# Kernel tuning notes

Measured on AMD Instinct MI355X. Metric: run time of the kernel, lower is better.

The kernel has to match this reference:

```python
import jax, jax.numpy as jnp
import numpy as np

EPS = 1e-05
HEADS = 4

def rms_norm(x, w):
    norm = jax.lax.rsqrt(jnp.mean(x * x, axis=-1, keepdims=True) + EPS)
    return x * norm * w

def setup_inputs() -> dict:
    key = jax.random.key(0)
    ks = jax.random.split(key, 10)
    B, Nt, Nf, C = 2, 4096, 4096, 256
    s = 0.02
    return {
        "t": jax.random.normal(ks[0], (B, Nt, C), jnp.float32),
        "f": jax.random.normal(ks[1], (B, Nf, C), jnp.float32),
        "norm_w": jnp.ones((C,), jnp.float32),
        "wq": jax.random.normal(ks[2], (C, C), jnp.float32) * s,
        "bq": jnp.zeros((C,), jnp.float32),
        "wkv": jax.random.normal(ks[3], (C, 2 * C), jnp.float32) * s,
        "bkv": jnp.zeros((2 * C,), jnp.float32),
        "wp": jax.random.normal(ks[4], (C, C), jnp.float32) * s,
        "bp": jnp.zeros((C,), jnp.float32),
    }

def reference(t, f, norm_w, wq, bq, wkv, bkv, wp, bp):
    B, Nt, C = t.shape
    Nf = f.shape[1]
    H = HEADS
    Dh = C // H
    scale = Dh ** -0.5
    tn = rms_norm(t, norm_w)
    fn = rms_norm(f, norm_w)
    q = (tn @ wq + bq).reshape(B, Nt, H, Dh)          # b t h d
    kv = fn @ wkv + bkv
    k, v = jnp.split(kv, 2, axis=-1)
    k = k.reshape(B, Nf, H, Dh)                        # b f h d
    v = v.reshape(B, Nf, H, Dh)
    attn = jnp.einsum('bthd,bfhd->bhtf', q, k) * scale
    attn = jax.nn.softmax(attn, axis=-1)
    out = jnp.einsum('bhtf,bfhd->bthd', attn, v).reshape(B, Nt, C)
    return out @ wp + bp + tn
```

## Files before the change

### kernel.cpp

```cpp
#include <hip/hip_runtime.h>

typedef __bf16 bf16;
typedef __bf16 bf16x4 __attribute__((ext_vector_type(4)));
typedef __bf16 bf16x8 __attribute__((ext_vector_type(8)));
typedef float f32x2 __attribute__((ext_vector_type(2)));
typedef float f32x4 __attribute__((ext_vector_type(4)));
typedef float f32x16 __attribute__((ext_vector_type(16)));

__device__ __forceinline__ f32x4 mfma16(bf16x8 a, bf16x8 b, f32x4 c) {
  return __builtin_amdgcn_mfma_f32_16x16x32_bf16(a, b, c, 0, 0, 0);
}
__device__ __forceinline__ f32x16 mfma32(bf16x8 a, bf16x8 b, f32x16 c) {
  return __builtin_amdgcn_mfma_f32_32x32x16_bf16(a, b, c, 0, 0, 0);
}

__device__ __forceinline__ unsigned pack2(float lo, float hi) {
  unsigned short a = __builtin_bit_cast(unsigned short, (bf16)lo);
  unsigned short b = __builtin_bit_cast(unsigned short, (bf16)hi);
  return ((unsigned)b << 16) | (unsigned)a;
}

__device__ __forceinline__ unsigned cvtpk(float lo, float hi) {
  unsigned r;
  asm("v_cvt_pk_bf16_f32 %0, %1, %2" : "=v"(r) : "v"(lo), "v"(hi));
  return r;
}

__device__ __forceinline__ void plane32swap(unsigned& a, unsigned& b) {
  asm volatile("v_permlane32_swap_b32 %0, %1" : "+v"(a), "+v"(b));
}

__device__ __forceinline__ f32x2 pk_add(f32x2 a, f32x2 b) {
  f32x2 d;
  asm("v_pk_add_f32 %0, %1, %2" : "=v"(d) : "v"(a), "v"(b));
  return d;
}

typedef __attribute__((address_space(3))) unsigned int lds_u32;
typedef __attribute__((address_space(1))) unsigned int glb_u32;
__device__ __forceinline__ void gld16(const bf16* g, bf16* l) {
  __builtin_amdgcn_global_load_lds((const glb_u32*)g, (lds_u32*)l, 16, 0, 0);
}

__global__ __launch_bounds__(256)
void prep_kernel(const float* __restrict__ t, const float* __restrict__ f,
                 const float* __restrict__ nw,
                 const float* __restrict__ wq, const float* __restrict__ wkv,
                 const float* __restrict__ wp,
                 bf16* __restrict__ tn, bf16* __restrict__ fn,
                 bf16* __restrict__ wqT, bf16* __restrict__ wkvT,
                 bf16* __restrict__ wpT)
{
  int b = blockIdx.x;
  if (b < 1024) {
    int e = b * 256 + threadIdx.x;
    const float* src; bf16* dst; int N; int idx;
    if (e < 65536)       { src = wq;  dst = wqT;  N = 256; idx = e; }
    else if (e < 196608) { src = wkv; dst = wkvT; N = 512; idx = e - 65536; }
    else                 { src = wp;  dst = wpT;  N = 256; idx = e - 196608; }
    int k = idx & 255;
    int n = idx >> 8;
    dst[idx] = (bf16)src[(size_t)k * N + n];
    return;
  }
  int wave = threadIdx.x >> 6;
  int lane = threadIdx.x & 63;
  int row = (b - 1024) * 4 + wave;
  const float* src;
  bf16* dst;
  if (row < 8192) {
    src = t + (size_t)row * 256;
    dst = tn + (size_t)row * 256;
  } else {
    int r2 = row - 8192;
    src = f + (size_t)r2 * 256;
    dst = fn + (size_t)r2 * 256;
  }
  float4 v = reinterpret_cast<const float4*>(src)[lane];
  float ss = v.x * v.x + v.y * v.y + v.z * v.z + v.w * v.w;
  #pragma unroll
  for (int m = 1; m < 64; m <<= 1) ss += __shfl_xor(ss, m);
  float nrm = rsqrtf(ss * (1.0f / 256.0f) + 1e-5f);
  float4 wv = reinterpret_cast<const float4*>(nw)[lane];
  bf16x4 o;
  o[0] = (bf16)(v.x * nrm * wv.x);
  o[1] = (bf16)(v.y * nrm * wv.y);
  o[2] = (bf16)(v.z * nrm * wv.z);
  o[3] = (bf16)(v.w * nrm * wv.w);
  *reinterpret_cast<bf16x4*>(dst + lane * 4) = o;
}

template<int MODE>
__device__ __forceinline__
void gemm_body(int bid, bf16 (*As)[264], bf16 (*Bs)[264],
               const bf16* __restrict__ A, const bf16* __restrict__ Wt,
               const float* __restrict__ bias, bf16* __restrict__ o0,
               bf16* __restrict__ o1, const bf16* __restrict__ resid,
               float* __restrict__ outf, int N)
{
  int tid = threadIdx.x;
  int wv = tid >> 6;
  int lane = tid & 63;
  int lr = lane & 15;
  int lk = (lane >> 4) * 8;
  int wm = wv >> 1, wn = wv & 1;
  int nb = N >> 6;
  int bm = bid / nb;
  int bn = bid - bm * nb;
  int row0 = bm * 64;
  int col0 = bn * 64;

  #pragma unroll
  for (int j = 0; j < 8; j++) {
    int idx = tid + 256 * j;
    int r = idx >> 5, ch = idx & 31;
    *reinterpret_cast<bf16x8*>(&As[r][ch * 8]) =
        *reinterpret_cast<const bf16x8*>(A + (size_t)(row0 + r) * 256 + ch * 8);
    *reinterpret_cast<bf16x8*>(&Bs[r][ch * 8]) =
        *reinterpret_cast<const bf16x8*>(Wt + (size_t)(col0 + r) * 256 + ch * 8);
  }
  __syncthreads();

  f32x4 acc[2][2] = {};
  #pragma unroll
  for (int k0 = 0; k0 < 256; k0 += 32) {
    bf16x8 a[2], b[2];
    #pragma unroll
    for (int mi = 0; mi < 2; mi++)
      a[mi] = *reinterpret_cast<const bf16x8*>(&As[wm * 32 + mi * 16 + lr][k0 + lk]);
    #pragma unroll
    for (int ni = 0; ni < 2; ni++)
      b[ni] = *reinterpret_cast<const bf16x8*>(&Bs[wn * 32 + ni * 16 + lr][k0 + lk]);
    #pragma unroll
    for (int mi = 0; mi < 2; mi++)
      #pragma unroll
      for (int ni = 0; ni < 2; ni++)
        acc[mi][ni] = mfma16(a[mi], b[ni], acc[mi][ni]);
  }

  int rb = (lane >> 4) * 4;
  int row0w = row0 + wm * 32;
  int col0w = col0 + wn * 32;
  #pragma unroll
  for (int mi = 0; mi < 2; mi++) {
    #pragma unroll
    for (int ni = 0; ni < 2; ni++) {
      int col = col0w + ni * 16 + lr;
      float bv = bias[col];
      #pragma unroll
      for (int r = 0; r < 4; r++) {
        int row = row0w + mi * 16 + rb + r;
        float val = acc[mi][ni][r] + bv;
        if (MODE == 0) {
          int b_ = row >> 12, tt = row & 4095;
          int h = col >> 6, d = col & 63;
          o0[(((size_t)(b_ * 4 + h)) * 4096 + tt) * 64 + d] = (bf16)val;
        } else if (MODE == 1) {
          int b_ = row >> 12, ff = row & 4095;
          if (col < 256) {
            int h = col >> 6, d = col & 63;
            o0[(((size_t)(b_ * 4 + h)) * 4096 + ff) * 64 + d] = (bf16)val;
          } else {
            int c = col - 256;
            int h = c >> 6, d = c & 63;
            o1[(((size_t)(b_ * 4 + h)) * 64 + d) * 4096 + ff] = (bf16)val;
          }
        } else {
          size_t idx = (size_t)row * 256 + col;
          outf[idx] = val + (float)resid[idx];
        }
      }
    }
  }
}

__global__ __launch_bounds__(256)
void gemm_qkv(const bf16* __restrict__ tn, const bf16* __restrict__ fn,
              const bf16* __restrict__ wqT, const bf16* __restrict__ wkvT,
              const float* __restrict__ bq, const float* __restrict__ bkv,
              bf16* __restrict__ q, bf16* __restrict__ k, bf16* __restrict__ vt)
{
  __shared__ bf16 As[64][264];
  __shared__ bf16 Bs[64][264];
  if (blockIdx.x < 512)
    gemm_body<0>(blockIdx.x, As, Bs, tn, wqT, bq, q, nullptr, nullptr, nullptr, 256);
  else
    gemm_body<1>(blockIdx.x - 512, As, Bs, fn, wkvT, bkv, k, vt, nullptr, nullptr, 512);
}

__global__ __launch_bounds__(256)
void gemm_out(const bf16* __restrict__ ao, const bf16* __restrict__ wpT,
              const float* __restrict__ bp, const bf16* __restrict__ resid,
              float* __restrict__ outf)
{
  __shared__ bf16 As[64][264];
  __shared__ bf16 Bs[64][264];
  gemm_body<2>(blockIdx.x, As, Bs, ao, wpT, bp, nullptr, nullptr, resid, outf, 256);
}

__global__ __launch_bounds__(256, 4)
void attn_kernel(const bf16* __restrict__ Q, const bf16* __restrict__ K,
                 const bf16* __restrict__ Vt, unsigned* __restrict__ Opart,
                 float* __restrict__ Lp)
{
  int bid = blockIdx.x;
  int bh = bid & 7;
  int qb = (bid >> 3) & 31;
  int FQ = bid >> 8;
  int wv = threadIdx.x >> 6;
  int lane = threadIdx.x & 63;
  int lq = lane & 31;
  int h32 = lane >> 5;

  const bf16* Qb = Q + ((size_t)bh * 4096 + qb * 128 + wv * 32) * 64;
  const bf16* Kb = K + (size_t)bh * 4096 * 64;
  const bf16* Vb = Vt + (size_t)bh * 64 * 4096;

  __shared__ bf16 stage[2][4096];

  const float qs = 0.125f * 1.44269504089f;
  bf16x8 qf[4];
  #pragma unroll
  for (int kc = 0; kc < 4; kc++) {
    qf[kc] = *reinterpret_cast<const bf16x8*>(Qb + (size_t)lq * 64 + kc * 16 + h32 * 8);
    #pragma unroll
    for (int i = 0; i < 8; i++) qf[kc][i] = (bf16)((float)qf[kc][i] * qs);
  }

  f32x16 oa[2] = {};
  f32x2 l2 = {0.f, 0.f};

  int fbeg = FQ * 512;

  int role = wv >> 1;
  int half = wv & 1;
  const bf16 *p0, *p1;
  if (role == 0) {
    p0 = Kb + (size_t)(fbeg + lq) * 64 + h32 * 8 + half * 32;
    p1 = p0 + 32 * 64;
  } else {
    p0 = Vb + (size_t)lane * 4096 + fbeg + half * 16;
    p1 = p0 + 32;
  }
  const int so  = role ? 8 : 16;
  const int adv = role ? 64 : 64 * 64;
  const int db0 = wv * 1024;

  const bf16* kL0 = &stage[0][0] + h32 * 256 + lq * 8;
  const bf16* kL1 = &stage[1][0] + h32 * 256 + lq * 8;
  const bf16* vL0 = &stage[0][2048] + h32 * 512 + lq * 8;
  const bf16* vL1 = &stage[1][2048] + h32 * 512 + lq * 8;

  auto STAGE = [&](bf16* sb, const bf16* p) {
    gld16(p,      sb + db0);
    gld16(p + so, sb + db0 + 512);
  };

  auto QK = [&](const bf16* kL) -> f32x16 {
    f32x16 z = {};
    f32x16 st = mfma32(*reinterpret_cast<const bf16x8*>(kL),        qf[0], z);
    st        = mfma32(*reinterpret_cast<const bf16x8*>(kL + 512),  qf[1], st);
    st        = mfma32(*reinterpret_cast<const bf16x8*>(kL + 1024), qf[2], st);
    st        = mfma32(*reinterpret_cast<const bf16x8*>(kL + 1536), qf[3], st);
    return st;
  };

  auto SMPV = [&](f32x16 st, const bf16* vL) {
    union { f32x2 p2[8]; float s[16]; } u;
    #pragma unroll
    for (int r = 0; r < 16; r++) u.s[r] = exp2f(st[r]);

    f32x2 a0 = pk_add(u.p2[0], u.p2[1]);
    f32x2 a1 = pk_add(u.p2[2], u.p2[3]);
    f32x2 a2 = pk_add(u.p2[4], u.p2[5]);
    f32x2 a3 = pk_add(u.p2[6], u.p2[7]);
    a0 = pk_add(a0, a1);
    a2 = pk_add(a2, a3);
    a0 = pk_add(a0, a2);
    l2 = pk_add(l2, a0);

    unsigned w[8];
    #pragma unroll
    for (int j = 0; j < 8; j++) w[j] = cvtpk(u.s[2 * j], u.s[2 * j + 1]);
    plane32swap(w[0], w[2]);
    plane32swap(w[1], w[3]);
    plane32swap(w[4], w[6]);
    plane32swap(w[5], w[7]);
    union { unsigned u4[4]; bf16x8 v; } ub0, ub1;
    ub0.u4[0] = w[0]; ub0.u4[1] = w[1]; ub0.u4[2] = w[2]; ub0.u4[3] = w[3];
    ub1.u4[0] = w[4]; ub1.u4[1] = w[5]; ub1.u4[2] = w[6]; ub1.u4[3] = w[7];

    oa[0] = mfma32(*reinterpret_cast<const bf16x8*>(vL),        ub0.v, oa[0]);
    oa[0] = mfma32(*reinterpret_cast<const bf16x8*>(vL + 1024), ub1.v, oa[0]);
    oa[1] = mfma32(*reinterpret_cast<const bf16x8*>(vL + 256),  ub0.v, oa[1]);
    oa[1] = mfma32(*reinterpret_cast<const bf16x8*>(vL + 1280), ub1.v, oa[1]);
  };

  STAGE(&stage[0][0], p0);
  STAGE(&stage[1][0], p1);
  asm volatile("" ::: "memory");

  #pragma unroll 1
  for (int u = 0; u < 8; ++u) {
    asm volatile("s_waitcnt vmcnt(0)" ::: "memory");
    __builtin_amdgcn_s_barrier();
    asm volatile("" ::: "memory");

    f32x16 sa = QK(kL0);
    f32x16 sb = QK(kL1);
    SMPV(sa, vL0);
    SMPV(sb, vL1);

    asm volatile("" ::: "memory");
    __builtin_amdgcn_s_barrier();
    asm volatile("" ::: "memory");

    p0 += adv;
    p1 += adv;
    STAGE(&stage[0][0], p0);
    STAGE(&stage[1][0], p1);
    asm volatile("" ::: "memory");
  }

  asm volatile("s_waitcnt vmcnt(0)" ::: "memory");

  float l = l2[0] + l2[1];
  float ltot;
  {
    unsigned x = __builtin_bit_cast(unsigned, l), y = x;
    plane32swap(x, y);
    ltot = __builtin_bit_cast(float, x) + __builtin_bit_cast(float, y);
  }

  int tile = qb * 4 + wv;
  unsigned* op = Opart + (((size_t)(FQ * 8 + bh) * 128 + tile) * 1024);
  #pragma unroll
  for (int db = 0; db < 2; db++)
    #pragma unroll
    for (int j = 0; j < 8; j++) {
      int r = 2 * j;
      int d = db * 32 + 2 * (j & 1) + 8 * (j >> 1) + 4 * h32;
      op[(d >> 1) * 32 + lq] = cvtpk(oa[db][r], oa[db][r + 1]);
    }
  if (h32 == 0)
    Lp[((size_t)FQ * 8 + bh) * 4096 + tile * 32 + lq] = ltot;
}

__global__ __launch_bounds__(256)
void merge_kernel(const unsigned* __restrict__ Op, const float* __restrict__ Lp,
                  bf16* __restrict__ AO)
{
  int bid = blockIdx.x;
  int bh = bid & 7;
  int tile = bid >> 3;
  int tid = threadIdx.x;
  int q = tid & 31;
  int c4 = tid >> 5;
  int row0 = tile * 32;

  float L = 0.f;
  #pragma unroll
  for (int p = 0; p < 8; p++)
    L += Lp[((size_t)p * 8 + bh) * 4096 + row0 + q];
  float inv = 1.f / L;

  __shared__ unsigned tl[32][33];
  float a0[4] = {}, a1[4] = {};
  #pragma unroll
  for (int p = 0; p < 8; p++) {
    const unsigned* src = Op + (((size_t)p * 8 + bh) * 128 + tile) * 1024;
    #pragma unroll
    for (int j = 0; j < 4; j++) {
      unsigned v = src[(c4 + j * 8) * 32 + q];
      a0[j] += (float)__builtin_bit_cast(bf16, (unsigned short)(v & 0xffff));
      a1[j] += (float)__builtin_bit_cast(bf16, (unsigned short)(v >> 16));
    }
  }
  #pragma unroll
  for (int j = 0; j < 4; j++)
    tl[q][c4 + j * 8] = pack2(a0[j] * inv, a1[j] * inv);
  __syncthreads();

  int q2 = tid >> 3;
  int dg = tid & 7;
  unsigned ov[4];
  #pragma unroll
  for (int i = 0; i < 4; i++) ov[i] = tl[q2][dg * 4 + i];
  int b_ = bh >> 2, hh = bh & 3;
  int row = row0 + q2;
  unsigned* dst = (unsigned*)(AO + ((size_t)b_ * 4096 + row) * 256 + hh * 64) + dg * 4;
  *reinterpret_cast<uint4*>(dst) = *reinterpret_cast<const uint4*>(ov);
}

extern "C" void kernel_launch(void* const* d_in, const int* in_sizes, int n_in,
                              void* d_out, int out_size, void* d_ws, size_t ws_size,
                              hipStream_t stream) {
  const float* t   = (const float*)d_in[0];
  const float* f   = (const float*)d_in[1];
  const float* nw  = (const float*)d_in[2];
  const float* wq  = (const float*)d_in[3];
  const float* bq  = (const float*)d_in[4];
  const float* wkv = (const float*)d_in[5];
  const float* bkv = (const float*)d_in[6];
  const float* wp  = (const float*)d_in[7];
  const float* bp  = (const float*)d_in[8];
  float* out = (float*)d_out;

  bf16* ws = (bf16*)d_ws;
  const size_t NTOK = 2097152;
  bf16* tn   = ws;
  bf16* fn   = ws + NTOK;
  bf16* q    = ws + 2 * NTOK;
  bf16* k    = ws + 3 * NTOK;
  bf16* vt   = ws + 4 * NTOK;
  bf16* ao   = fn;
  bf16* wqT  = ws + 5 * NTOK;
  bf16* wkvT = wqT + 65536;
  bf16* wpT  = wkvT + 131072;
  unsigned* opart = (unsigned*)(wpT + 65536);
  float* lp = (float*)(opart + (size_t)8 * 8 * 128 * 1024);

  prep_kernel<<<5120, 256, 0, stream>>>(t, f, nw, wq, wkv, wp, tn, fn, wqT, wkvT, wpT);
  gemm_qkv<<<1536, 256, 0, stream>>>(tn, fn, wqT, wkvT, bq, bkv, q, k, vt);
  attn_kernel<<<2048, 256, 0, stream>>>(q, k, vt, opart, lp);
  merge_kernel<<<1024, 256, 0, stream>>>(opart, lp, ao);
  gemm_out<<<512, 256, 0, stream>>>(ao, wpT, bp, tn, out);
}
```

Baseline: 100.0 us.

## Double-buffer K/V shared-memory staging to overlap global loads with compute

Shared staging grows from two to four buffers, split into two pairs that alternate. While one pair is consumed by QK/softmax/PV, the loads for the other pair stay in flight, and the wait becomes vmcnt(4) instead of vmcnt(0). This is meant to hide global-to-LDS load latency behind MFMA work, but it doubles LDS per block to 32KB, which may reduce occupancy under launch bounds of 4 blocks per CU.

```diff
diff --git a/kernel.cpp b/kernel.cpp
--- a/kernel.cpp
+++ b/kernel.cpp
@@ -216,7 +216,7 @@
   const bf16* Kb = K + (size_t)bh * 4096 * 64;
   const bf16* Vb = Vt + (size_t)bh * 64 * 4096;
 
-  __shared__ bf16 stage[2][4096];
+  __shared__ bf16 stage[4][4096];
 
   const float qs = 0.125f * 1.44269504089f;
   bf16x8 qf[4];
@@ -234,26 +234,32 @@
 
   int role = wv >> 1;
   int half = wv & 1;
-  const bf16 *p0, *p1;
+  const bf16 *pA, *pB;
   if (role == 0) {
-    p0 = Kb + (size_t)(fbeg + lq) * 64 + h32 * 8 + half * 32;
-    p1 = p0 + 32 * 64;
+    pA = Kb + (size_t)(fbeg + lq) * 64 + h32 * 8 + half * 32;
+    pB = pA + 64 * 64;
   } else {
-    p0 = Vb + (size_t)lane * 4096 + fbeg + half * 16;
-    p1 = p0 + 32;
+    pA = Vb + (size_t)lane * 4096 + fbeg + half * 16;
+    pB = pA + 64;
   }
   const int so  = role ? 8 : 16;
-  const int adv = role ? 64 : 64 * 64;
+  const int to  = role ? 32 : 32 * 64;
+  const int adv = role ? 128 : 128 * 64;
   const int db0 = wv * 1024;
 
-  const bf16* kL0 = &stage[0][0] + h32 * 256 + lq * 8;
-  const bf16* kL1 = &stage[1][0] + h32 * 256 + lq * 8;
-  const bf16* vL0 = &stage[0][2048] + h32 * 512 + lq * 8;
-  const bf16* vL1 = &stage[1][2048] + h32 * 512 + lq * 8;
-
-  auto STAGE = [&](bf16* sb, const bf16* p) {
-    gld16(p,      sb + db0);
-    gld16(p + so, sb + db0 + 512);
+  const bf16* kLb[4];
+  const bf16* vLb[4];
+  #pragma unroll
+  for (int b = 0; b < 4; b++) {
+    kLb[b] = &stage[b][0] + h32 * 256 + lq * 8;
+    vLb[b] = &stage[b][2048] + h32 * 512 + lq * 8;
+  }
+
+  auto STAGEPAIR = [&](int b0, const bf16* p) {
+    gld16(p,           &stage[b0][0] + db0);
+    gld16(p + so,      &stage[b0][0] + db0 + 512);
+    gld16(p + to,      &stage[b0 + 1][0] + db0);
+    gld16(p + to + so, &stage[b0 + 1][0] + db0 + 512);
   };
 
   auto QK = [&](const bf16* kL) -> f32x16 {
@@ -296,30 +302,33 @@
     oa[1] = mfma32(*reinterpret_cast<const bf16x8*>(vL + 1280), ub1.v, oa[1]);
   };
 
-  STAGE(&stage[0][0], p0);
-  STAGE(&stage[1][0], p1);
-  asm volatile("" ::: "memory");
-
-  #pragma unroll 1
-  for (int u = 0; u < 8; ++u) {
-    asm volatile("s_waitcnt vmcnt(0)" ::: "memory");
+  auto REGION = [&](int b0, const bf16*& p) {
+    asm volatile("s_waitcnt vmcnt(4)" ::: "memory");
     __builtin_amdgcn_s_barrier();
     asm volatile("" ::: "memory");
 
-    f32x16 sa = QK(kL0);
-    f32x16 sb = QK(kL1);
-    SMPV(sa, vL0);
-    SMPV(sb, vL1);
+    f32x16 sa = QK(kLb[b0]);
+    f32x16 sb = QK(kLb[b0 + 1]);
+    SMPV(sa, vLb[b0]);
+    SMPV(sb, vLb[b0 + 1]);
 
     asm volatile("" ::: "memory");
     __builtin_amdgcn_s_barrier();
     asm volatile("" ::: "memory");
 
-    p0 += adv;
-    p1 += adv;
-    STAGE(&stage[0][0], p0);
-    STAGE(&stage[1][0], p1);
+    p += adv;
+    STAGEPAIR(b0, p);
     asm volatile("" ::: "memory");
+  };
+
+  STAGEPAIR(0, pA);
+  STAGEPAIR(2, pB);
+  asm volatile("" ::: "memory");
+
+  #pragma unroll 1
+  for (int u = 0; u < 4; ++u) {
+    REGION(0, pA);
+    REGION(2, pB);
   }
 
   asm volatile("s_waitcnt vmcnt(0)" ::: "memory");
```

Result: no change. 98.23 us (-1.8%).
